# Performance work log

Measured on AMD Instinct MI355X. Metric: run time of the kernel, lower is better.

Reference implementation:

```python
import jax, jax.numpy as jnp
import numpy as np


def setup_inputs() -> dict:
    key = jax.random.key(0)
    k1, k2, k3 = jax.random.split(key, 3)
    B, L, D, C = 4, 4096, 1024, 1
    x = jax.random.normal(k1, (B, L, D), dtype=jnp.float32)
    kernel = jax.random.normal(k2, (C, D, L), dtype=jnp.float32)
    Dskip = jax.random.normal(k3, (C, D), dtype=jnp.float32)
    return {"x": x, "kernel": kernel, "D": Dskip}


def reference(x, kernel, D):
    # x: [B, L, H]  kernel: [C, H, L]  D: [C, H]
    L = x.shape[1]
    n = 2 * L
    xt = jnp.transpose(x, (0, 2, 1))  # [B, H, L]
    # soft-threshold the kernel: relu(|k| - 0.1) * sign(k)
    k = jax.nn.relu(jnp.abs(kernel) - 0.1) * jnp.sign(kernel)
    k_f = jnp.fft.rfft(k, n=n)          # [C, H, n//2+1] complex
    x_f = jnp.fft.rfft(xt, n=n)         # [B, H, n//2+1] complex
    y_f = jnp.einsum('bhl,chl->bchl', x_f, k_f)
    y = jnp.fft.irfft(y_f, n=n)[..., :L]            # [B, C, H, L]
    y = y + jnp.einsum('bhl,ch->bchl', xt, D)        # skip term
    # rearrange 'b c h l -> b l (c h)'
    Bn, Cn, Hn, Ln = y.shape
    return jnp.transpose(y, (0, 3, 1, 2)).reshape(Bn, Ln, Cn * Hn)
```

## Files before the change

### kernel.cpp

```cpp
#include <hip/hip_runtime.h>


typedef __attribute__((ext_vector_type(8)))  short s16x8;
typedef __attribute__((ext_vector_type(16))) float f32x16;
typedef __attribute__((ext_vector_type(4)))  float f32x4;
typedef __attribute__((ext_vector_type(4)))  unsigned int u32x4;

constexpr int B_ = 4, L_ = 4096, H_ = 1024;
constexpr int PADX = 256;
constexpr int LX = L_ + PADX;
constexpr int LK = L_ + 32;
constexpr int ST = 256;
constexpr int NST = L_ / ST;

constexpr size_t XT_ELEMS = (size_t)B_ * H_ * LX;
constexpr size_t KR_ELEMS = (size_t)2 * H_ * LK;
constexpr size_t OT_ELEMS = (size_t)B_ * H_ * L_;
constexpr size_t WS_NEEDED = (XT_ELEMS + KR_ELEMS + OT_ELEMS) * sizeof(unsigned short);

constexpr int XS_ROW  = 4320;
constexpr int XS_BLKS = XS_ROW / 8;
constexpr int XS_US   = B_ * XS_ROW;
constexpr int KS_US   = 2 * LK;
constexpr int OAREA_DW = 4 * 132;
constexpr int SMEM_MAIN = XS_US * 2 + KS_US * 2;

constexpr int nHt = H_ / 64, nLt = L_ / 64;
constexpr int NXB = B_ * nLt * nHt;
constexpr int nLt2 = L_ / 128;
constexpr int NUT = B_ * nLt2 * nHt;

__device__ __forceinline__ unsigned short f2bf(float f) {
    unsigned int u = __builtin_bit_cast(unsigned int, f);
    u += 0x7fffu + ((u >> 16) & 1u);
    return (unsigned short)(u >> 16);
}
__device__ __forceinline__ float bf2f(unsigned short u) {
    return __builtin_bit_cast(float, (unsigned int)u << 16);
}
__device__ __forceinline__ unsigned int sw16(unsigned int x) {
    return (x >> 16) | (x << 16);
}

__global__ __launch_bounds__(256)
void prep(const float* __restrict__ x, const float* __restrict__ kin,
          const float* __restrict__ Dk,
          unsigned short* __restrict__ xT, unsigned short* __restrict__ kR)
{
    __shared__ __align__(16) unsigned char pshm[16704];
    const int bid = blockIdx.x;
    if (bid < NXB) {
        float (*tile)[65] = (float (*)[65])pshm;
        const int b  = bid / (nLt * nHt);
        const int r0 = bid % (nLt * nHt);
        const int l0 = (r0 / nHt) * 64;
        const int h0 = (r0 % nHt) * 64;
        const int j  = threadIdx.x;
        const int h4 = j & 15;
        const int rg = j >> 4;
        #pragma unroll
        for (int it = 0; it < 4; ++it) {
            const int lr = rg + 16 * it;
            const f32x4 v = *(const f32x4*)(x + ((size_t)b * L_ + l0 + lr) * H_ + h0 + 4 * h4);
            tile[lr][4 * h4 + 0] = v.x; tile[lr][4 * h4 + 1] = v.y;
            tile[lr][4 * h4 + 2] = v.z; tile[lr][4 * h4 + 3] = v.w;
        }
        __syncthreads();
        const int lg = j & 7;
        #pragma unroll
        for (int pp = 0; pp < 2; ++pp) {
            const int hh = (j >> 3) + 32 * pp;
            unsigned int w0 = (unsigned int)f2bf(tile[8*lg+0][hh]) | ((unsigned int)f2bf(tile[8*lg+1][hh]) << 16);
            unsigned int w1 = (unsigned int)f2bf(tile[8*lg+2][hh]) | ((unsigned int)f2bf(tile[8*lg+3][hh]) << 16);
            unsigned int w2 = (unsigned int)f2bf(tile[8*lg+4][hh]) | ((unsigned int)f2bf(tile[8*lg+5][hh]) << 16);
            unsigned int w3 = (unsigned int)f2bf(tile[8*lg+6][hh]) | ((unsigned int)f2bf(tile[8*lg+7][hh]) << 16);
            const u32x4 v = {w0, w1, w2, w3};
            *(u32x4*)(xT + ((size_t)b * H_ + h0 + hh) * LX + PADX + l0 + 8 * lg) = v;
        }
        if (l0 == 0) {
            #pragma unroll
            for (int it = 0; it < 8; ++it) {
                const int idx = j + 256 * it;
                const int row = idx >> 5, off = idx & 31;
                const u32x4 z = {};
                *(u32x4*)(xT + ((size_t)b * H_ + h0 + row) * LX + off * 8) = z;
            }
        }
    } else {
        unsigned short* kb0 = (unsigned short*)pshm;
        unsigned short* kb1 = kb0 + 4144;
        const int h = bid - NXB;
        const int j = threadIdx.x;
        const float Dv = Dk[h];
        if (j < 40) { kb0[j] = 0; kb1[j] = 0; }
        const float* kh = kin + (size_t)h * L_;
        float vv[17];
        {
            const int l0 = 16 * j;
            float am = (j > 0) ? kh[l0 - 1] : 0.0f;
            vv[0] = copysignf(fmaxf(fabsf(am) - 0.1f, 0.0f), am);
            #pragma unroll
            for (int g = 0; g < 4; ++g) {
                const f32x4 a = *(const f32x4*)(kh + l0 + 4 * g);
                vv[1 + 4*g + 0] = copysignf(fmaxf(fabsf(a.x) - 0.1f, 0.0f), a.x);
                vv[1 + 4*g + 1] = copysignf(fmaxf(fabsf(a.y) - 0.1f, 0.0f), a.y);
                vv[1 + 4*g + 2] = copysignf(fmaxf(fabsf(a.z) - 0.1f, 0.0f), a.z);
                vv[1 + 4*g + 3] = copysignf(fmaxf(fabsf(a.w) - 0.1f, 0.0f), a.w);
            }
            if (j == 0) vv[1] += Dv;
        }
        {
            unsigned int d0[8], d1[8];
            #pragma unroll
            for (int g = 0; g < 8; ++g) {
                d0[g] = (unsigned int)f2bf(vv[1 + 2*g]) | ((unsigned int)f2bf(vv[2 + 2*g]) << 16);
                d1[g] = (unsigned int)f2bf(vv[0 + 2*g]) | ((unsigned int)f2bf(vv[1 + 2*g]) << 16);
            }
            u32x4* p0 = (u32x4*)(kb0 + 40 + 16 * j);
            u32x4* p1 = (u32x4*)(kb1 + 40 + 16 * j);
            p0[0] = u32x4{d0[0], d0[1], d0[2], d0[3]};
            p0[1] = u32x4{d0[4], d0[5], d0[6], d0[7]};
            p1[0] = u32x4{d1[0], d1[1], d1[2], d1[3]};
            p1[1] = u32x4{d1[4], d1[5], d1[6], d1[7]};
        }
        __syncthreads();
        for (int v = j; v < LK / 8; v += 256) {
            const u32x4 a0 = *(const u32x4*)(kb0 + 4128 - 8 * v);
            const u32x4 a1 = *(const u32x4*)(kb1 + 4128 - 8 * v);
            const u32x4 r0 = {sw16(a0.w), sw16(a0.z), sw16(a0.y), sw16(a0.x)};
            const u32x4 r1 = {sw16(a1.w), sw16(a1.z), sw16(a1.y), sw16(a1.x)};
            *(u32x4*)(kR + (size_t)h * LK + 8 * v) = r0;
            *(u32x4*)(kR + ((size_t)H_ + h) * LK + 8 * v) = r1;
        }
    }
}

#define BODY(DO0, DO1, DO2, DO3)                                            \
  {                                                                         \
    _Pragma("unroll")                                                       \
    for (int i = 0; i < 16; ++i) {                                          \
      u32x4 aw;                                                             \
      aw.x = abase[8*i+0]; aw.y = abase[8*i+1];                             \
      aw.z = abase[8*i+2]; aw.w = abase[8*i+3];                             \
      const s16x8 af = __builtin_bit_cast(s16x8, aw);                       \
      const int io = 32 * (i >> 1);                                         \
      if (DO3) acc3 = __builtin_amdgcn_mfma_f32_32x32x16_bf16(              \
            af, *(const s16x8*)(((i & 1) ? t3b : t3a) + io), acc3, 0,0,0);  \
      if (DO2) acc2 = __builtin_amdgcn_mfma_f32_32x32x16_bf16(              \
            af, *(const s16x8*)(((i & 1) ? t2b : t2a) + io), acc2, 0,0,0);  \
      if (DO1) acc1 = __builtin_amdgcn_mfma_f32_32x32x16_bf16(              \
            af, *(const s16x8*)(((i & 1) ? t1b : t1a) + io), acc1, 0,0,0);  \
      if (DO0) acc0 = __builtin_amdgcn_mfma_f32_32x32x16_bf16(              \
            af, *(const s16x8*)(((i & 1) ? t0b : t0a) + io), acc0, 0,0,0);  \
    }                                                                       \
    abase -= 128;                                                           \
    if (DO3) { t3a -= 256; t3b -= 256; }                                    \
    if (DO2) { t2a -= 256; t2b -= 256; }                                    \
    if (DO1) { t1a -= 256; t1b -= 256; }                                    \
    if (DO0) { t0a -= 256; t0b -= 256; }                                    \
  }

__global__ __launch_bounds__(256, 2)
void longconv_main(const unsigned short* __restrict__ xT,
                   const unsigned short* __restrict__ kR,
                   unsigned int* __restrict__ outT)
{
    __shared__ __align__(16) unsigned char smem[SMEM_MAIN];
    unsigned short* xs = (unsigned short*)smem;
    unsigned short* ks = (unsigned short*)(smem + (size_t)XS_US * 2);

    const int h   = blockIdx.x;
    const int tid = threadIdx.x;

    constexpr int NXU = XS_BLKS * 4;
    constexpr int NKU = 2 * (LK / 8);
    for (int u = tid; u < NXU + NKU; u += 256) {
        if (u < NXU) {
            const int b = u / XS_BLKS, n = u - b * XS_BLKS;
            const u32x4 v = *(const u32x4*)(xT + ((size_t)b * H_ + h) * LX + 32 + n * 8);
            *(u32x4*)(xs + (size_t)b * XS_ROW + (size_t)(n ^ b) * 8) = v;
        } else {
            const int v2 = u - NXU;
            const int p = v2 / (LK / 8), i = v2 - p * (LK / 8);
            const u32x4 v = *(const u32x4*)(kR + ((size_t)p * H_ + h) * LK + i * 8);
            *(u32x4*)(ks + (size_t)p * LK + (size_t)i * 8) = v;
        }
    }
    __syncthreads();

    const int w  = tid >> 6, ln = tid & 63;
    const int m  = ln & 31,  q  = ln >> 5;
    const int t  = m >> 2,   b  = m & 3;
    const int si0 = w, si1 = 7 - w, si2 = 8 + w, si3 = 15 - w;

    const int base = 3871 - m + 8 * q;
    const int p    = base & 1;
    const unsigned int* abase = (const unsigned int*)(ks + p * LK + (base - p));
    const unsigned short* xrow = xs + (size_t)b * XS_ROW;
    const int nb = 4 * t + q;

    auto mk = [&](int si, int par) -> const unsigned short* {
        const int n = 32 * si + nb + 2 * par;
        return xrow + (size_t)((n ^ b) * 8);
    };
    const unsigned short *t0a = mk(si0, 0), *t0b = mk(si0, 1);
    const unsigned short *t1a = mk(si1, 0), *t1b = mk(si1, 1);
    const unsigned short *t2a = mk(si2, 0), *t2b = mk(si2, 1);
    const unsigned short *t3a = mk(si3, 0), *t3b = mk(si3, 1);

    f32x16 acc0 = {}, acc1 = {}, acc2 = {}, acc3 = {};
    int beta = 0;
    for (; beta <= si0; ++beta) BODY(1, 1, 1, 1);
    for (; beta <= si1; ++beta) BODY(0, 1, 1, 1);
    for (; beta <= si2; ++beta) BODY(0, 0, 1, 1);
    for (; beta <= si3; ++beta) BODY(0, 0, 0, 1);

    __syncthreads();
    float* oarea = (float*)smem;
    float* ar = oarea + w * OAREA_DW;
    auto writeout = [&](const f32x16& acc, int si) {
        const int Ls = si * ST;
        #pragma unroll
        for (int rh = 0; rh < 2; ++rh) {
            #pragma unroll
            for (int rr2 = 0; rr2 < 2; ++rr2) {
                const int base4 = (8 * rr2 + 4 * q + 4 * t) & 15;
                f32x4 qd;
                qd.x = acc[4 * (2 * rh + rr2) + 0];
                qd.y = acc[4 * (2 * rh + rr2) + 1];
                qd.z = acc[4 * (2 * rh + rr2) + 2];
                qd.w = acc[4 * (2 * rh + rr2) + 3];
                *(f32x4*)(ar + b * 132 + 16 * t + base4) = qd;
            }
            __asm__ volatile("s_waitcnt lgkmcnt(0)" ::: "memory");
            #pragma unroll
            for (int bb = 0; bb < 4; ++bb) {
                const int g  = ln >> 3;
                const int uu = (2 * ln) & 15;
                const int s  = (uu + 4 * g) & 15;
                const float v0 = ar[bb * 132 + 16 * g + s];
                const float v1 = ar[bb * 132 + 16 * g + s + 1];
                const int l = 32 * g + 16 * rh + uu;
                const unsigned int pk =
                    (unsigned int)f2bf(v0) | ((unsigned int)f2bf(v1) << 16);
                outT[(((size_t)bb * H_ + h) * L_ + Ls + l) >> 1] = pk;
            }
            __asm__ volatile("s_waitcnt lgkmcnt(0)" ::: "memory");
        }
    };
    writeout(acc0, si0);
    writeout(acc1, si1);
    writeout(acc2, si2);
    writeout(acc3, si3);
}

__global__ __launch_bounds__(256)
void untranspose(const unsigned short* __restrict__ outT, float* __restrict__ out)
{
    __shared__ __align__(16) float tile[128][68];
    const int bid = blockIdx.x;
    const int b  = bid / (nLt2 * nHt);
    const int r0 = bid % (nLt2 * nHt);
    const int l0 = (r0 / nHt) * 128;
    const int h0 = (r0 % nHt) * 64;
    const int j  = threadIdx.x;
    const int lg = j & 7;
    u32x4 v[2][2];
    #pragma unroll
    for (int tt = 0; tt < 2; ++tt)
        #pragma unroll
        for (int pp = 0; pp < 2; ++pp) {
            const int hh = (j >> 3) + 32 * pp;
            v[tt][pp] = *(const u32x4*)(outT + ((size_t)b * H_ + h0 + hh) * L_
                                        + l0 + 64 * tt + 8 * lg);
        }
    #pragma unroll
    for (int tt = 0; tt < 2; ++tt)
        #pragma unroll
        for (int pp = 0; pp < 2; ++pp) {
            const int hh = (j >> 3) + 32 * pp;
            const unsigned short* pu = (const unsigned short*)&v[tt][pp];
            #pragma unroll
            for (int i = 0; i < 8; ++i) {
                const int row = 64 * tt + 8 * lg + i;
                tile[row][hh ^ (4 * lg)] = bf2f(pu[i]);
            }
        }
    __syncthreads();
    const int hg = j & 15;
    #pragma unroll
    for (int pz = 0; pz < 8; ++pz) {
        const int ll = (j >> 4) + 16 * pz;
        const f32x4 vv = *(const f32x4*)(&tile[ll][4 * (hg ^ ((ll >> 3) & 7))]);
        *(f32x4*)(out + ((size_t)b * L_ + l0 + ll) * H_ + h0 + 4 * hg) = vv;
    }
}

constexpr int TLf = 32, Uf = 8, Wf = TLf + Uf - 1, HTf = 256;

__global__ __launch_bounds__(HTf)
void longconv_fp32(const float* __restrict__ x, const float* __restrict__ k,
                   const float* __restrict__ Dskip, float* __restrict__ out)
{
    const int h  = blockIdx.y * HTf + threadIdx.x;
    const int b  = blockIdx.z;
    const int lt = (int)gridDim.x - 1 - (int)blockIdx.x;
    const int L0 = lt * TLf;
    const float* __restrict__ xb = x + ((size_t)b * L_) * H_ + h;
    const float* __restrict__ kh = k + (size_t)h * L_;
    float acc[TLf]; float win[Wf];
    #pragma unroll
    for (int i = 0; i < Wf; ++i) {
        const int idx = L0 - (Uf - 1) + i;
        win[i] = (idx >= 0) ? xb[(size_t)idx * H_] : 0.0f;
    }
    const float Dv = Dskip[h];
    #pragma unroll
    for (int jj = 0; jj < TLf; ++jj) acc[jj] = win[jj + Uf - 1] * Dv;
    const int cmax = L0 / Uf + (TLf / Uf) - 1;
    for (int c = 0; c <= cmax; ++c) {
        float kr[Uf];
        #pragma unroll
        for (int u = 0; u < Uf; ++u) {
            const float a = kh[c * Uf + u];
            kr[u] = copysignf(fmaxf(fabsf(a) - 0.1f, 0.0f), a);
        }
        #pragma unroll
        for (int u = 0; u < Uf; ++u)
            #pragma unroll
            for (int jj = 0; jj < TLf; ++jj)
                acc[jj] = fmaf(kr[u], win[jj + (Uf - 1) - u], acc[jj]);
        if (c < cmax) {
            #pragma unroll
            for (int i = Wf - 1; i >= Uf; --i) win[i] = win[i - Uf];
            #pragma unroll
            for (int i = 0; i < Uf; ++i) {
                const int idx = L0 - (c + 1) * Uf - (Uf - 1) + i;
                win[i] = (idx >= 0) ? xb[(size_t)idx * H_] : 0.0f;
            }
        }
    }
    float* __restrict__ ob = out + ((size_t)b * L_ + L0) * H_ + h;
    #pragma unroll
    for (int jj = 0; jj < TLf; ++jj) ob[(size_t)jj * H_] = acc[jj];
}

extern "C" void kernel_launch(void* const* d_in, const int* in_sizes, int n_in,
                              void* d_out, int out_size, void* d_ws, size_t ws_size,
                              hipStream_t stream)
{
    const float* x  = (const float*)d_in[0];
    const float* k  = (const float*)d_in[1];
    const float* Dk = (const float*)d_in[2];
    float* out = (float*)d_out;

    if (ws_size >= WS_NEEDED) {
        unsigned short* xT = (unsigned short*)d_ws;
        unsigned short* kR = xT + XT_ELEMS;
        unsigned short* oT = kR + KR_ELEMS;
        prep<<<dim3(NXB + H_), dim3(256), 0, stream>>>(x, k, Dk, xT, kR);
        longconv_main<<<dim3(H_), dim3(256), 0, stream>>>(xT, kR, (unsigned int*)oT);
        untranspose<<<dim3(NUT), dim3(256), 0, stream>>>(oT, out);
    } else {
        dim3 grid(L_ / TLf, H_ / HTf, B_);
        longconv_fp32<<<grid, dim3(HTf), 0, stream>>>(x, k, Dk, out);
    }
}
```

Baseline: 211.2 us.

## Assign contiguous output tiles per wave to reuse x fragments across MFMAs

Each wave now owns four consecutive 256-sample output tiles instead of a balanced mirrored set. The main loop processes two kernel blocks at once and shares five loaded x fragments across eight MFMAs, which cuts LDS reads per MFMA. A short triangular tail handles the remaining blocks. Work is no longer balanced across the four waves: wave w does roughly 4w+... blocks, so the last wave dominates, which may lengthen the critical path.

```diff
diff --git a/kernel.cpp b/kernel.cpp
--- a/kernel.cpp
+++ b/kernel.cpp
@@ -135,30 +135,7 @@
     }
 }
 
-#define BODY(DO0, DO1, DO2, DO3)                                            \
-  {                                                                         \
-    _Pragma("unroll")                                                       \
-    for (int i = 0; i < 16; ++i) {                                          \
-      u32x4 aw;                                                             \
-      aw.x = abase[8*i+0]; aw.y = abase[8*i+1];                             \
-      aw.z = abase[8*i+2]; aw.w = abase[8*i+3];                             \
-      const s16x8 af = __builtin_bit_cast(s16x8, aw);                       \
-      const int io = 32 * (i >> 1);                                         \
-      if (DO3) acc3 = __builtin_amdgcn_mfma_f32_32x32x16_bf16(              \
-            af, *(const s16x8*)(((i & 1) ? t3b : t3a) + io), acc3, 0,0,0);  \
-      if (DO2) acc2 = __builtin_amdgcn_mfma_f32_32x32x16_bf16(              \
-            af, *(const s16x8*)(((i & 1) ? t2b : t2a) + io), acc2, 0,0,0);  \
-      if (DO1) acc1 = __builtin_amdgcn_mfma_f32_32x32x16_bf16(              \
-            af, *(const s16x8*)(((i & 1) ? t1b : t1a) + io), acc1, 0,0,0);  \
-      if (DO0) acc0 = __builtin_amdgcn_mfma_f32_32x32x16_bf16(              \
-            af, *(const s16x8*)(((i & 1) ? t0b : t0a) + io), acc0, 0,0,0);  \
-    }                                                                       \
-    abase -= 128;                                                           \
-    if (DO3) { t3a -= 256; t3b -= 256; }                                    \
-    if (DO2) { t2a -= 256; t2b -= 256; }                                    \
-    if (DO1) { t1a -= 256; t1b -= 256; }                                    \
-    if (DO0) { t0a -= 256; t0b -= 256; }                                    \
-  }
+#define MFMA_BF16 __builtin_amdgcn_mfma_f32_32x32x16_bf16
 
 __global__ __launch_bounds__(256, 2)
 void longconv_main(const unsigned short* __restrict__ xT,
@@ -191,7 +168,6 @@
     const int w  = tid >> 6, ln = tid & 63;
     const int m  = ln & 31,  q  = ln >> 5;
     const int t  = m >> 2,   b  = m & 3;
-    const int si0 = w, si1 = 7 - w, si2 = 8 + w, si3 = 15 - w;
 
     const int base = 3871 - m + 8 * q;
     const int p    = base & 1;
@@ -199,21 +175,63 @@
     const unsigned short* xrow = xs + (size_t)b * XS_ROW;
     const int nb = 4 * t + q;
 
-    auto mk = [&](int si, int par) -> const unsigned short* {
-        const int n = 32 * si + nb + 2 * par;
-        return xrow + (size_t)((n ^ b) * 8);
-    };
-    const unsigned short *t0a = mk(si0, 0), *t0b = mk(si0, 1);
-    const unsigned short *t1a = mk(si1, 0), *t1b = mk(si1, 1);
-    const unsigned short *t2a = mk(si2, 0), *t2b = mk(si2, 1);
-    const unsigned short *t3a = mk(si3, 0), *t3b = mk(si3, 1);
+    const unsigned short* X0a = xrow + (size_t)(((nb + 0) ^ b) * 8);
+    const unsigned short* X0b = xrow + (size_t)(((nb + 2) ^ b) * 8);
 
     f32x16 acc0 = {}, acc1 = {}, acc2 = {}, acc3 = {};
-    int beta = 0;
-    for (; beta <= si0; ++beta) BODY(1, 1, 1, 1);
-    for (; beta <= si1; ++beta) BODY(0, 1, 1, 1);
-    for (; beta <= si2; ++beta) BODY(0, 0, 1, 1);
-    for (; beta <= si3; ++beta) BODY(0, 0, 0, 1);
+
+    const unsigned short* sXa = X0a + (4 * w - 1) * 256;
+    const unsigned short* sXb = X0b + (4 * w - 1) * 256;
+    for (int sb = 0; sb < 2 * w; ++sb) {
+        const unsigned int* abaseP = abase - 128;
+        #pragma unroll
+        for (int i = 0; i < 16; ++i) {
+            u32x4 a0, a1;
+            a0.x = abase[8*i+0];  a0.y = abase[8*i+1];
+            a0.z = abase[8*i+2];  a0.w = abase[8*i+3];
+            a1.x = abaseP[8*i+0]; a1.y = abaseP[8*i+1];
+            a1.z = abaseP[8*i+2]; a1.w = abaseP[8*i+3];
+            const s16x8 af0 = __builtin_bit_cast(s16x8, a0);
+            const s16x8 af1 = __builtin_bit_cast(s16x8, a1);
+            const unsigned short* xp = ((i & 1) ? sXb : sXa) + 32 * (i >> 1);
+            const s16x8 x0 = *(const s16x8*)(xp);
+            const s16x8 x1 = *(const s16x8*)(xp + 256);
+            const s16x8 x2 = *(const s16x8*)(xp + 512);
+            const s16x8 x3 = *(const s16x8*)(xp + 768);
+            const s16x8 x4 = *(const s16x8*)(xp + 1024);
+            acc0 = MFMA_BF16(af0, x1, acc0, 0,0,0);
+            acc0 = MFMA_BF16(af1, x0, acc0, 0,0,0);
+            acc1 = MFMA_BF16(af0, x2, acc1, 0,0,0);
+            acc1 = MFMA_BF16(af1, x1, acc1, 0,0,0);
+            acc2 = MFMA_BF16(af0, x3, acc2, 0,0,0);
+            acc2 = MFMA_BF16(af1, x2, acc2, 0,0,0);
+            acc3 = MFMA_BF16(af0, x4, acc3, 0,0,0);
+            acc3 = MFMA_BF16(af1, x3, acc3, 0,0,0);
+        }
+        abase -= 256; sXa -= 512; sXb -= 512;
+    }
+
+#define TAILBODY(D0, D1, D2, D3, O0, O1, O2, O3)                            \
+  {                                                                         \
+    _Pragma("unroll")                                                       \
+    for (int i = 0; i < 16; ++i) {                                          \
+      u32x4 aw;                                                             \
+      aw.x = abase[8*i+0]; aw.y = abase[8*i+1];                             \
+      aw.z = abase[8*i+2]; aw.w = abase[8*i+3];                             \
+      const s16x8 af = __builtin_bit_cast(s16x8, aw);                       \
+      const unsigned short* xp = ((i & 1) ? X0b : X0a) + 32 * (i >> 1);     \
+      if (D0) acc0 = MFMA_BF16(af, *(const s16x8*)(xp + O0), acc0, 0,0,0);  \
+      if (D1) acc1 = MFMA_BF16(af, *(const s16x8*)(xp + O1), acc1, 0,0,0);  \
+      if (D2) acc2 = MFMA_BF16(af, *(const s16x8*)(xp + O2), acc2, 0,0,0);  \
+      if (D3) acc3 = MFMA_BF16(af, *(const s16x8*)(xp + O3), acc3, 0,0,0);  \
+    }                                                                       \
+    abase -= 128;                                                           \
+  }
+    TAILBODY(1, 1, 1, 1, 0, 256, 512, 768);
+    TAILBODY(0, 1, 1, 1, 0, 0,   256, 512);
+    TAILBODY(0, 0, 1, 1, 0, 0,   0,   256);
+    TAILBODY(0, 0, 0, 1, 0, 0,   0,   0  );
+#undef TAILBODY
 
     __syncthreads();
     float* oarea = (float*)smem;
@@ -248,10 +266,10 @@
             __asm__ volatile("s_waitcnt lgkmcnt(0)" ::: "memory");
         }
     };
-    writeout(acc0, si0);
-    writeout(acc1, si1);
-    writeout(acc2, si2);
-    writeout(acc3, si3);
+    writeout(acc0, 4 * w + 0);
+    writeout(acc1, 4 * w + 1);
+    writeout(acc2, 4 * w + 2);
+    writeout(acc3, 4 * w + 3);
 }
 
 __global__ __launch_bounds__(256)
```

Result: slower. 217.6 us (+3.0%).
